# Optimization experiments

Measured on AMD Instinct MI355X. Metric: run time of the kernel, lower is better.

The kernel has to match this reference:

```python
import jax, jax.numpy as jnp
import numpy as np

H = 256           # lstm_hidden_dim
D_IN = 22         # input_dim
H1, H2, H3 = 1024, 512, 1024
RRI = 2
N_R = N_L = 384


def _lstm_dir(x, Wih, Whh, b, reverse):
    # x: [T, D]; Wih: [4H, D]; Whh: [4H, H]; b: [4H] (bih+bhh). PyTorch gate order i,f,g,o.
    xs = x[::-1] if reverse else x
    pre = xs @ Wih.T + b                       # [T, 4H] input projection hoisted out of scan
    hdim = Whh.shape[1]

    def step(carry, p):
        h, c = carry
        g = p + h @ Whh.T
        i, f, gg, o = jnp.split(g, 4)
        i = jax.nn.sigmoid(i); f = jax.nn.sigmoid(f)
        gg = jnp.tanh(gg); o = jax.nn.sigmoid(o)
        c = f * c + i * gg
        h = o * jnp.tanh(c)
        return (h, c), h

    h0 = jnp.zeros((hdim,), x.dtype)
    _, hs = jax.lax.scan(step, (h0, h0), pre)
    return hs[::-1] if reverse else hs


def _bilstm(x, Wih0, Whh0, bih0, bhh0, Wih1, Whh1, bih1, bhh1):
    # 2-layer bidirectional LSTM (dropout between layers is identity in eval).
    b0 = bih0 + bhh0
    x1 = jnp.concatenate([_lstm_dir(x, Wih0[0], Whh0[0], b0[0], False),
                          _lstm_dir(x, Wih0[1], Whh0[1], b0[1], True)], axis=-1)
    b1 = bih1 + bhh1
    return jnp.concatenate([_lstm_dir(x1, Wih1[0], Whh1[0], b1[0], False),
                            _lstm_dir(x1, Wih1[1], Whh1[1], b1[1], True)], axis=-1)


def _mlp(h, W1, b1, W2, b2):
    h1 = jax.nn.relu(h @ W1.T + b1)
    return jax.nn.relu(h1 @ W2.T + b2)   # [N, H2]


def setup_inputs() -> dict:
    key = jax.random.key(0)
    ks = jax.random.split(key, 20)
    s = 0.05
    f = lambda k, shp: (jax.random.normal(k, shp, dtype=jnp.float32) * s)
    return {
        "v_r": jax.random.normal(ks[0], (N_R, D_IN), dtype=jnp.float32),
        "v_l": jax.random.normal(ks[1], (N_L, D_IN), dtype=jnp.float32),
        # LSTM layer 0 (input D_IN), stacked over 2 directions
        "Wih0": f(ks[2], (2, 4 * H, D_IN)),
        "Whh0": f(ks[3], (2, 4 * H, H)),
        "bih0": f(ks[4], (2, 4 * H)),
        "bhh0": f(ks[5], (2, 4 * H)),
        # LSTM layer 1 (input 2H)
        "Wih1": f(ks[6], (2, 4 * H, 2 * H)),
        "Whh1": f(ks[7], (2, 4 * H, H)),
        "bih1": f(ks[8], (2, 4 * H)),
        "bhh1": f(ks[9], (2, 4 * H)),
        # MLP heads
        "W1": f(ks[10], (H1, 2 * H)), "b1": f(ks[11], (H1,)),
        "W2": f(ks[12], (H2, H1)),    "b2": f(ks[13], (H2,)),
        "W3": f(ks[14], (H3, 2 * H2)), "b3": f(ks[15], (H3,)),
        "Wout": f(ks[16], (RRI, H3)), "bout": f(ks[17], (RRI,)),
    }


def reference(v_r, v_l, Wih0, Whh0, bih0, bhh0, Wih1, Whh1, bih1, bhh1,
              W1, b1, W2, b2, W3, b3, Wout, bout):
    out_r = _bilstm(v_r, Wih0, Whh0, bih0, bhh0, Wih1, Whh1, bih1, bhh1)  # [Nr, 2H]
    out_l = _bilstm(v_l, Wih0, Whh0, bih0, bhh0, Wih1, Whh1, bih1, bhh1)  # [Nl, 2H]
    hr = _mlp(out_r, W1, b1, W2, b2)   # [Nr, H2]
    hl = _mlp(out_l, W1, b1, W2, b2)   # [Nl, H2]
    # Original: 0.5*(Linear3([hr_i, hl_j]) + Linear3([hl_j, hr_i])) built via huge
    # repeat()s; exactly equal to u_r[i] + u_l[j] + b3 with the split weight sum.
    d2 = hr.shape[-1]
    W3s = (W3[:, :d2] + W3[:, d2:]).T            # [H2, H3]
    u_r = 0.5 * (hr @ W3s)                       # [Nr, H3]
    u_l = 0.5 * (hl @ W3s)                       # [Nl, H3]
    conv = jax.nn.relu(u_r[:, None, :] + u_l[None, :, :] + b3)  # [Nr, Nl, H3]
    v_in = conv.reshape(-1, conv.shape[-1])      # [Nr*Nl, H3], i_r-major like the torch loop
    logits = v_in @ Wout.T + bout                # [Nr*Nl, rri_size]
    return jax.nn.log_softmax(logits, axis=-1)
```

## Files before the change

### kernel.cpp

```cpp
#include <hip/hip_runtime.h>
#include <math.h>


typedef _Float16 half2_t __attribute__((ext_vector_type(2)));

__device__ __forceinline__ float fast_sig(float x) {
    float e = __expf(-x);
    return __builtin_amdgcn_rcpf(1.f + e);
}
__device__ __forceinline__ float fast_tanh(float x) {
    x = fminf(fmaxf(x, -30.f), 30.f);
    float e = __expf(2.f * x);
    return (e - 1.f) * __builtin_amdgcn_rcpf(e + 1.f);
}

__global__ __launch_bounds__(256) void prep_kernel(
    const float* __restrict__ bih0, const float* __restrict__ bhh0,
    const float* __restrict__ bih1, const float* __restrict__ bhh1,
    const float* __restrict__ W3,   const float* __restrict__ Wout,
    float* __restrict__ b0sum, float* __restrict__ b1sum,
    float* __restrict__ W3sum, float* __restrict__ woutT)
{
    int idx = blockIdx.x * 256 + threadIdx.x;
    int stride = gridDim.x * 256;
    if (idx < 2048) {
        b0sum[idx] = bih0[idx] + bhh0[idx];
        b1sum[idx] = bih1[idx] + bhh1[idx];
        woutT[idx] = Wout[(idx & 1) * 1024 + (idx >> 1)];
    }
    for (int i = idx; i < 1024 * 512; i += stride) {
        int n = i >> 9, k = i & 511;
        W3sum[i] = W3[n * 1024 + k] + W3[n * 1024 + 512 + k];
    }
}

__global__ __launch_bounds__(256) void proj0_kernel(
    const float* __restrict__ v_r, const float* __restrict__ v_l,
    const float* __restrict__ Wih0, const float* __restrict__ b0sum,
    float* __restrict__ pre0)
{
    int t = blockIdx.x;
    int sd = blockIdx.y;
    int seq = sd >> 1, dir = sd & 1;
    const float* x = (seq ? v_l : v_r) + t * 22;
    __shared__ float sx[22];
    if (threadIdx.x < 22) sx[threadIdx.x] = x[threadIdx.x];
    __syncthreads();
#pragma unroll
    for (int q = 0; q < 4; ++q) {
        int o = q * 256 + threadIdx.x;
        const float* wr = Wih0 + (size_t)(dir * 1024 + o) * 22;
        float acc = b0sum[dir * 1024 + o];
#pragma unroll
        for (int d = 0; d < 22; ++d) acc += sx[d] * wr[d];
        pre0[((size_t)sd * 384 + t) * 1024 + o] = acc;
    }
}

__global__ __launch_bounds__(512, 2) void lstm_rec_kernel(
    const float* __restrict__ Whh,
    const float* __restrict__ pre,
    float* __restrict__ out,
    unsigned long long* pub,
    int layer)
{
    const int b = blockIdx.x;
    const int chain = b & 7;
    const int w = b >> 3;
    if (chain >= 4) return;
    const int seq = chain >> 1, dir = chain & 1;
    const int tid = threadIdx.x;
    const int ks = tid & 3;
    const int r = tid >> 2;
    const int j = (w << 7) + r;

    __shared__ half2_t hh[4 * 40];
    __shared__ float gbuf[512];

    float wt[4][32];
#pragma unroll
    for (int g = 0; g < 4; ++g) {
        const float* wrow = Whh + (((size_t)(dir * 1024 + g * 256 + j)) << 8) + (ks << 6);
#pragma unroll
        for (int q = 0; q < 32; ++q) {
            float2 v = *(const float2*)(wrow + 2 * q);
            half2_t h2;
            h2.x = (_Float16)v.x;
            h2.y = (_Float16)v.y;
            wt[g][q] = __builtin_bit_cast(float, h2);
        }
    }
#pragma unroll
    for (int g = 0; g < 4; ++g)
#pragma unroll
        for (int q = 0; q < 32; ++q)
            asm volatile("" : "+v"(wt[g][q]));

    if (tid < 160) hh[tid] = half2_t{(_Float16)0.f, (_Float16)0.f};
    float cstate = 0.f;
    __syncthreads();

    for (int s = 0; s < 384; ++s) {
        const int t = dir ? (383 - s) : s;
        const float* pre_t = (layer == 0)
            ? pre + ((size_t)(seq * 2 + dir) * 384 + t) * 1024
            : pre + (((size_t)(seq * 384 + t)) * 2 + dir) * 1024;
        float pg0 = 0.f, pg1 = 0.f, pg2 = 0.f, pg3 = 0.f;
        if (tid < 128) {
            const int jw = (w << 7) + tid;
            pg0 = pre_t[jw];
            pg1 = pre_t[256 + jw];
            pg2 = pre_t[512 + jw];
            pg3 = pre_t[768 + jw];
        }

        float4 hl[8];
        {
            const float4* hb4 = (const float4*)(hh + 40 * ks);
#pragma unroll
            for (int m = 0; m < 8; ++m) hl[m] = hb4[m];
        }
        float a0 = 0.f, a1 = 0.f, a2 = 0.f, a3 = 0.f;
#pragma unroll
        for (int m = 0; m < 8; ++m) {
            const float he[4] = {hl[m].x, hl[m].y, hl[m].z, hl[m].w};
#pragma unroll
            for (int e = 0; e < 4; ++e) {
                half2_t hv = __builtin_bit_cast(half2_t, he[e]);
                int q = 4 * m + e;
                a0 = __builtin_amdgcn_fdot2(__builtin_bit_cast(half2_t, wt[0][q]), hv, a0, false);
                a1 = __builtin_amdgcn_fdot2(__builtin_bit_cast(half2_t, wt[1][q]), hv, a1, false);
                a2 = __builtin_amdgcn_fdot2(__builtin_bit_cast(half2_t, wt[2][q]), hv, a2, false);
                a3 = __builtin_amdgcn_fdot2(__builtin_bit_cast(half2_t, wt[3][q]), hv, a3, false);
            }
        }
#pragma unroll
        for (int d = 1; d < 4; d <<= 1) {
            a0 += __shfl_xor(a0, d);
            a1 += __shfl_xor(a1, d);
            a2 += __shfl_xor(a2, d);
            a3 += __shfl_xor(a3, d);
        }
        if (ks == 0) {
            gbuf[r]       = a0;
            gbuf[128 + r] = a1;
            gbuf[256 + r] = a2;
            gbuf[384 + r] = a3;
        }
        __syncthreads();

        unsigned long long* pb = pub + ((size_t)chain * 2 + (s & 1)) * 128;
        if (tid < 128) {
            const int jw = (w << 7) + tid;
            float iv = fast_sig(gbuf[tid] + pg0);
            float fv = fast_sig(gbuf[128 + tid] + pg1);
            float gv = fast_tanh(gbuf[256 + tid] + pg2);
            float ov = fast_sig(gbuf[384 + tid] + pg3);
            cstate = fv * cstate + iv * gv;
            float h = ov * fast_tanh(cstate);
            _Float16 hf = (_Float16)h;
            unsigned hb = (unsigned)__builtin_bit_cast(unsigned short, hf);
            {
                int p = jw >> 1;
                int slot = 40 * (p >> 5) + (p & 31);
                ((__attribute__((address_space(3))) unsigned short*)hh)[2 * slot + (jw & 1)] =
                    (unsigned short)hb;
            }
            unsigned up = (unsigned)__shfl_xor((int)hb, 1);
            if ((tid & 1) == 0) {
                unsigned payload = hb | (up << 16);
                unsigned long long pk =
                    ((unsigned long long)(unsigned)(s + 1) << 32) | payload;
                __hip_atomic_store(&pb[(w << 6) + (tid >> 1)], pk,
                                   __ATOMIC_RELAXED, __HIP_MEMORY_SCOPE_AGENT);
            }
            out[((size_t)seq * 384 + t) * 512 + dir * 256 + jw] = h;
        } else if (tid >= 256 && tid < 320) {
            int p = tid - 256;
            int wp = 1 - w;
            const unsigned long long* src = &pb[(wp << 6) + p];
            const unsigned expect = (unsigned)(s + 1);
            unsigned long long v =
                __hip_atomic_load(src, __ATOMIC_RELAXED, __HIP_MEMORY_SCOPE_AGENT);
            if ((unsigned)(v >> 32) != expect) {
                for (int it = 0; it < 65536; ++it) {
                    __builtin_amdgcn_s_sleep(1);
                    v = __hip_atomic_load(src, __ATOMIC_RELAXED, __HIP_MEMORY_SCOPE_AGENT);
                    if ((unsigned)(v >> 32) == expect) break;
                }
            }
            int pp = (wp << 6) + p;
            hh[40 * (pp >> 5) + (pp & 31)] =
                __builtin_bit_cast(half2_t, (unsigned)v);
        }
        __syncthreads();
    }
}

__global__ __launch_bounds__(256) void gemm_nt_kernel(
    const float* __restrict__ A, const float* __restrict__ W,
    const float* __restrict__ bias, float* __restrict__ C,
    int M, int N, int K, float scale, int do_relu)
{
    __shared__ float As[32][68];
    __shared__ float Ws[32][68];
    const int tid = threadIdx.x;
    const int n0 = blockIdx.x * 64, m0 = blockIdx.y * 64;
    const int lr = tid >> 2;
    const int lk = (tid & 3) * 8;
    const int tm = tid >> 4, tn = tid & 15;
    float acc[4][4];
#pragma unroll
    for (int i = 0; i < 4; ++i)
#pragma unroll
        for (int j = 0; j < 4; ++j) acc[i][j] = 0.f;

    for (int kc = 0; kc < K; kc += 32) {
        float4 a0 = *(const float4*)(A + (size_t)(m0 + lr) * K + kc + lk);
        float4 a1 = *(const float4*)(A + (size_t)(m0 + lr) * K + kc + lk + 4);
        float4 w0 = *(const float4*)(W + (size_t)(n0 + lr) * K + kc + lk);
        float4 w1 = *(const float4*)(W + (size_t)(n0 + lr) * K + kc + lk + 4);
        __syncthreads();
        As[lk + 0][lr] = a0.x; As[lk + 1][lr] = a0.y; As[lk + 2][lr] = a0.z; As[lk + 3][lr] = a0.w;
        As[lk + 4][lr] = a1.x; As[lk + 5][lr] = a1.y; As[lk + 6][lr] = a1.z; As[lk + 7][lr] = a1.w;
        Ws[lk + 0][lr] = w0.x; Ws[lk + 1][lr] = w0.y; Ws[lk + 2][lr] = w0.z; Ws[lk + 3][lr] = w0.w;
        Ws[lk + 4][lr] = w1.x; Ws[lk + 5][lr] = w1.y; Ws[lk + 6][lr] = w1.z; Ws[lk + 7][lr] = w1.w;
        __syncthreads();
#pragma unroll
        for (int kk = 0; kk < 32; ++kk) {
            float4 av = *(const float4*)&As[kk][tm * 4];
            float4 wv = *(const float4*)&Ws[kk][tn * 4];
            acc[0][0] += av.x * wv.x; acc[0][1] += av.x * wv.y; acc[0][2] += av.x * wv.z; acc[0][3] += av.x * wv.w;
            acc[1][0] += av.y * wv.x; acc[1][1] += av.y * wv.y; acc[1][2] += av.y * wv.z; acc[1][3] += av.y * wv.w;
            acc[2][0] += av.z * wv.x; acc[2][1] += av.z * wv.y; acc[2][2] += av.z * wv.z; acc[2][3] += av.z * wv.w;
            acc[3][0] += av.w * wv.x; acc[3][1] += av.w * wv.y; acc[3][2] += av.w * wv.z; acc[3][3] += av.w * wv.w;
        }
    }
    float4 bv = make_float4(0.f, 0.f, 0.f, 0.f);
    if (bias) bv = *(const float4*)(bias + n0 + tn * 4);
#pragma unroll
    for (int i = 0; i < 4; ++i) {
        int m = m0 + tm * 4 + i;
        float4 v;
        v.x = scale * acc[i][0] + bv.x;
        v.y = scale * acc[i][1] + bv.y;
        v.z = scale * acc[i][2] + bv.z;
        v.w = scale * acc[i][3] + bv.w;
        if (do_relu) {
            v.x = fmaxf(v.x, 0.f); v.y = fmaxf(v.y, 0.f);
            v.z = fmaxf(v.z, 0.f); v.w = fmaxf(v.w, 0.f);
        }
        *(float4*)(C + (size_t)m * N + n0 + tn * 4) = v;
    }
}

__global__ __launch_bounds__(256) void pairwise_kernel(
    const float* __restrict__ u,
    const float* __restrict__ woutT,
    const float* __restrict__ bout,
    float* __restrict__ out)
{
    __shared__ float Ur[32][132];
    __shared__ float Ul[32][132];
    __shared__ float Wo[256];
    const int tid = threadIdx.x;
    const int j0 = blockIdx.x * 32, i0 = blockIdx.y * 32;
    const int ii = tid >> 4, jj = tid & 15;
    const int il0 = ii, il1 = ii + 16;
    const int jl0 = jj, jl1 = jj + 16;
    float acc000 = 0.f, acc001 = 0.f, acc010 = 0.f, acc011 = 0.f;
    float acc100 = 0.f, acc101 = 0.f, acc110 = 0.f, acc111 = 0.f;
    const int lrw = tid >> 3;
    const int lcb = (tid & 7) * 16;

    for (int cc = 0; cc < 1024; cc += 128) {
        __syncthreads();
#pragma unroll
        for (int q = 0; q < 4; ++q) {
            *(float4*)&Ur[lrw][lcb + 4 * q] =
                *(const float4*)(u + (size_t)(i0 + lrw) * 1024 + cc + lcb + 4 * q);
            *(float4*)&Ul[lrw][lcb + 4 * q] =
                *(const float4*)(u + (size_t)(384 + j0 + lrw) * 1024 + cc + lcb + 4 * q);
        }
        if (tid < 128)
            *(float2*)&Wo[tid * 2] = *(const float2*)(woutT + (size_t)(cc + tid) * 2);
        __syncthreads();

        for (int c = 0; c < 128; c += 4) {
            float4 a0  = *(const float4*)&Ur[il0][c];
            float4 a1  = *(const float4*)&Ur[il1][c];
            float4 b0v = *(const float4*)&Ul[jl0][c];
            float4 b1v = *(const float4*)&Ul[jl1][c];
            float4 wA4 = *(const float4*)&Wo[c * 2];
            float4 wB4 = *(const float4*)&Wo[c * 2 + 4];
#define PW_STEP(AX, W0, W1)                                   \
            { float rr;                                       \
              rr = fmaxf(a0.AX + b0v.AX, 0.f); acc000 += rr*(W0); acc001 += rr*(W1); \
              rr = fmaxf(a0.AX + b1v.AX, 0.f); acc010 += rr*(W0); acc011 += rr*(W1); \
              rr = fmaxf(a1.AX + b0v.AX, 0.f); acc100 += rr*(W0); acc101 += rr*(W1); \
              rr = fmaxf(a1.AX + b1v.AX, 0.f); acc110 += rr*(W0); acc111 += rr*(W1); }
            PW_STEP(x, wA4.x, wA4.y)
            PW_STEP(y, wA4.z, wA4.w)
            PW_STEP(z, wB4.x, wB4.y)
            PW_STEP(w, wB4.z, wB4.w)
#undef PW_STEP
        }
    }
    float2 bo = *(const float2*)bout;
    float pa[2][2][2] = {{{acc000, acc001}, {acc010, acc011}},
                         {{acc100, acc101}, {acc110, acc111}}};
#pragma unroll
    for (int pi = 0; pi < 2; ++pi)
#pragma unroll
        for (int pj = 0; pj < 2; ++pj) {
            float l0 = pa[pi][pj][0] + bo.x;
            float l1 = pa[pi][pj][1] + bo.y;
            float m = fmaxf(l0, l1);
            float lse = m + logf(expf(l0 - m) + expf(l1 - m));
            int ig = i0 + ii + 16 * pi;
            int jg = j0 + jj + 16 * pj;
            float2 o2; o2.x = l0 - lse; o2.y = l1 - lse;
            *(float2*)(out + ((size_t)ig * 384 + jg) * 2) = o2;
        }
}

extern "C" void kernel_launch(void* const* d_in, const int* in_sizes, int n_in,
                              void* d_out, int out_size, void* d_ws, size_t ws_size,
                              hipStream_t stream)
{
    const float* v_r  = (const float*)d_in[0];
    const float* v_l  = (const float*)d_in[1];
    const float* Wih0 = (const float*)d_in[2];
    const float* Whh0 = (const float*)d_in[3];
    const float* bih0 = (const float*)d_in[4];
    const float* bhh0 = (const float*)d_in[5];
    const float* Wih1 = (const float*)d_in[6];
    const float* Whh1 = (const float*)d_in[7];
    const float* bih1 = (const float*)d_in[8];
    const float* bhh1 = (const float*)d_in[9];
    const float* W1   = (const float*)d_in[10];
    const float* b1   = (const float*)d_in[11];
    const float* W2   = (const float*)d_in[12];
    const float* b2   = (const float*)d_in[13];
    const float* W3   = (const float*)d_in[14];
    const float* b3   = (const float*)d_in[15];
    const float* Wout = (const float*)d_in[16];
    const float* bout = (const float*)d_in[17];
    float* out = (float*)d_out;

    float* ws = (float*)d_ws;
    size_t off = 0;
    float* b0sum = ws + off; off += 2048;
    float* b1sum = ws + off; off += 2048;
    float* W3sum = ws + off; off += 1024 * 512;
    float* woutT = ws + off; off += 2048;
    float* pre0  = ws + off; off += (size_t)4 * 384 * 1024;
    float* out0  = ws + off; off += (size_t)2 * 384 * 512;
    float* pre1  = ws + off; off += (size_t)768 * 2048;
    float* out1  = ws + off; off += (size_t)2 * 384 * 512;
    float* h1    = ws + off; off += (size_t)768 * 1024;
    float* h2    = ws + off; off += (size_t)768 * 512;
    float* u     = ws + off; off += (size_t)768 * 1024;
    unsigned long long* pub0 = (unsigned long long*)(ws + off); off += 4 * 2 * 128 * 2;
    unsigned long long* pub1 = (unsigned long long*)(ws + off); off += 4 * 2 * 128 * 2;

    prep_kernel<<<512, 256, 0, stream>>>(bih0, bhh0, bih1, bhh1, W3, Wout,
                                         b0sum, b1sum, W3sum, woutT);
    proj0_kernel<<<dim3(384, 4), 256, 0, stream>>>(v_r, v_l, Wih0, b0sum, pre0);
    lstm_rec_kernel<<<16, 512, 0, stream>>>(Whh0, pre0, out0, pub0, 0);
    gemm_nt_kernel<<<dim3(2048 / 64, 768 / 64), 256, 0, stream>>>(
        out0, Wih1, b1sum, pre1, 768, 2048, 512, 1.f, 0);
    lstm_rec_kernel<<<16, 512, 0, stream>>>(Whh1, pre1, out1, pub1, 1);
    gemm_nt_kernel<<<dim3(1024 / 64, 768 / 64), 256, 0, stream>>>(
        out1, W1, b1, h1, 768, 1024, 512, 1.f, 1);
    gemm_nt_kernel<<<dim3(512 / 64, 768 / 64), 256, 0, stream>>>(
        h1, W2, b2, h2, 768, 512, 1024, 1.f, 1);
    gemm_nt_kernel<<<dim3(1024 / 64, 384 / 64), 256, 0, stream>>>(
        h2, W3sum, b3, u, 384, 1024, 512, 0.5f, 0);
    gemm_nt_kernel<<<dim3(1024 / 64, 384 / 64), 256, 0, stream>>>(
        h2 + (size_t)384 * 512, W3sum, nullptr, u + (size_t)384 * 1024, 384, 1024, 512, 0.5f, 0);
    pairwise_kernel<<<dim3(12, 12), 256, 0, stream>>>(u, woutT, bout, out);
}
```

Before: 1.411 ms.

## Remove per-step gate buffer barrier via shuffle-reduced gates and double-buffered h

The LSTM recurrence kernel no longer writes gate partial sums to shared memory and syncs before the cell update. Instead each 4-lane group adds its preactivation slice before the xor-shuffle reduction, so every lane holds all four gates and computes the cell redundantly. The hidden state is double-buffered in shared memory, which leaves one barrier per timestep instead of two. Publishing, output writes and polling of the partner workgroup's state are spread across different lanes. The cost is redundant transcendental work in every lane.

```diff
diff --git a/kernel.cpp b/kernel.cpp
--- a/kernel.cpp
+++ b/kernel.cpp
@@ -74,8 +74,7 @@
     const int r = tid >> 2;
     const int j = (w << 7) + r;
 
-    __shared__ half2_t hh[4 * 40];
-    __shared__ float gbuf[512];
+    __shared__ __align__(16) half2_t hh[2][160];
 
     float wt[4][32];
 #pragma unroll
@@ -96,8 +95,14 @@
         for (int q = 0; q < 32; ++q)
             asm volatile("" : "+v"(wt[g][q]));
 
-    if (tid < 160) hh[tid] = half2_t{(_Float16)0.f, (_Float16)0.f};
+    if (tid < 320) ((half2_t*)hh)[tid] = half2_t{(_Float16)0.f, (_Float16)0.f};
     float cstate = 0.f;
+
+    const bool isPub  = (ks == 0) && ((r & 1) == 0);
+    const bool isOut  = (ks == 1);
+    const bool isPoll = (ks == 3) && ((r & 1) == 1);
+    const int  p  = r >> 1;
+    const int  wp = 1 - w;
     __syncthreads();
 
     for (int s = 0; s < 384; ++s) {
@@ -105,21 +110,13 @@
         const float* pre_t = (layer == 0)
             ? pre + ((size_t)(seq * 2 + dir) * 384 + t) * 1024
             : pre + (((size_t)(seq * 384 + t)) * 2 + dir) * 1024;
-        float pg0 = 0.f, pg1 = 0.f, pg2 = 0.f, pg3 = 0.f;
-        if (tid < 128) {
-            const int jw = (w << 7) + tid;
-            pg0 = pre_t[jw];
-            pg1 = pre_t[256 + jw];
-            pg2 = pre_t[512 + jw];
-            pg3 = pre_t[768 + jw];
-        }
-
+        float pv = pre_t[(ks << 8) + j];
+
+        const float4* rb = (const float4*)(hh[s & 1] + 40 * ks);
         float4 hl[8];
-        {
-            const float4* hb4 = (const float4*)(hh + 40 * ks);
-#pragma unroll
-            for (int m = 0; m < 8; ++m) hl[m] = hb4[m];
-        }
+#pragma unroll
+        for (int m = 0; m < 8; ++m) hl[m] = rb[m];
+
         float a0 = 0.f, a1 = 0.f, a2 = 0.f, a3 = 0.f;
 #pragma unroll
         for (int m = 0; m < 8; ++m) {
@@ -134,6 +131,10 @@
                 a3 = __builtin_amdgcn_fdot2(__builtin_bit_cast(half2_t, wt[3][q]), hv, a3, false);
             }
         }
+        a0 += (ks == 0) ? pv : 0.f;
+        a1 += (ks == 1) ? pv : 0.f;
+        a2 += (ks == 2) ? pv : 0.f;
+        a3 += (ks == 3) ? pv : 0.f;
 #pragma unroll
         for (int d = 1; d < 4; d <<= 1) {
             a0 += __shfl_xor(a0, d);
@@ -141,44 +142,33 @@
             a2 += __shfl_xor(a2, d);
             a3 += __shfl_xor(a3, d);
         }
-        if (ks == 0) {
-            gbuf[r]       = a0;
-            gbuf[128 + r] = a1;
-            gbuf[256 + r] = a2;
-            gbuf[384 + r] = a3;
-        }
-        __syncthreads();
-
+
+        float iv = fast_sig(a0);
+        float fv = fast_sig(a1);
+        float gv = fast_tanh(a2);
+        float ov = fast_sig(a3);
+        cstate = fv * cstate + iv * gv;
+        float h = ov * fast_tanh(cstate);
+
+        unsigned hb = (unsigned)__builtin_bit_cast(unsigned short, (_Float16)h);
+        unsigned nb = (unsigned)__shfl_xor((int)hb, 4);
+        half2_t* wb = hh[(s + 1) & 1];
         unsigned long long* pb = pub + ((size_t)chain * 2 + (s & 1)) * 128;
-        if (tid < 128) {
-            const int jw = (w << 7) + tid;
-            float iv = fast_sig(gbuf[tid] + pg0);
-            float fv = fast_sig(gbuf[128 + tid] + pg1);
-            float gv = fast_tanh(gbuf[256 + tid] + pg2);
-            float ov = fast_sig(gbuf[384 + tid] + pg3);
-            cstate = fv * cstate + iv * gv;
-            float h = ov * fast_tanh(cstate);
-            _Float16 hf = (_Float16)h;
-            unsigned hb = (unsigned)__builtin_bit_cast(unsigned short, hf);
-            {
-                int p = jw >> 1;
-                int slot = 40 * (p >> 5) + (p & 31);
-                ((__attribute__((address_space(3))) unsigned short*)hh)[2 * slot + (jw & 1)] =
-                    (unsigned short)hb;
-            }
-            unsigned up = (unsigned)__shfl_xor((int)hb, 1);
-            if ((tid & 1) == 0) {
-                unsigned payload = hb | (up << 16);
-                unsigned long long pk =
-                    ((unsigned long long)(unsigned)(s + 1) << 32) | payload;
-                __hip_atomic_store(&pb[(w << 6) + (tid >> 1)], pk,
-                                   __ATOMIC_RELAXED, __HIP_MEMORY_SCOPE_AGENT);
-            }
-            out[((size_t)seq * 384 + t) * 512 + dir * 256 + jw] = h;
-        } else if (tid >= 256 && tid < 320) {
-            int p = tid - 256;
-            int wp = 1 - w;
-            const unsigned long long* src = &pb[(wp << 6) + p];
+
+        if (isPub) {
+            unsigned payload = (hb & 0xffffu) | (nb << 16);
+            int P = (w << 6) + p;
+            wb[40 * (P >> 5) + (P & 31)] = __builtin_bit_cast(half2_t, payload);
+            unsigned long long pk =
+                ((unsigned long long)(unsigned)(s + 1) << 32) | payload;
+            __hip_atomic_store(&pb[P], pk, __ATOMIC_RELAXED, __HIP_MEMORY_SCOPE_AGENT);
+        }
+        if (isOut) {
+            out[((size_t)seq * 384 + t) * 512 + dir * 256 + j] = h;
+        }
+        if (isPoll) {
+            int P = (wp << 6) + p;
+            const unsigned long long* src = &pb[P];
             const unsigned expect = (unsigned)(s + 1);
             unsigned long long v =
                 __hip_atomic_load(src, __ATOMIC_RELAXED, __HIP_MEMORY_SCOPE_AGENT);
@@ -189,9 +179,7 @@
                     if ((unsigned)(v >> 32) == expect) break;
                 }
             }
-            int pp = (wp << 6) + p;
-            hh[40 * (pp >> 5) + (pp & 31)] =
-                __builtin_bit_cast(half2_t, (unsigned)v);
+            wb[40 * (P >> 5) + (P & 31)] = __builtin_bit_cast(half2_t, (unsigned)v);
         }
         __syncthreads();
     }
```

Result: slower. 1.439 ms (+2.0%).
